# Optimization experiments

Hardware: AMD Instinct MI355X
Metric: run time of the kernel (lower is better)

## Reference

```python
import jax, jax.numpy as jnp
import numpy as np

CROSS_SIZES = [256, 256, 256]  # split_half=True -> carried field sizes [39,128,128,256]


def setup_inputs() -> dict:
    key = jax.random.key(0)
    ks = jax.random.split(key, 6)
    B, F, D = 1024, 39, 32
    scale = 0.05
    return {
        "x": jax.random.normal(ks[0], (B, F, D), dtype=jnp.float32),
        "W0": jax.random.normal(ks[1], (F * F, 256), dtype=jnp.float32) * scale,
        "b0": jnp.zeros((256,), dtype=jnp.float32),
        "W1": jax.random.normal(ks[2], (F * 128, 256), dtype=jnp.float32) * scale,
        "b1": jnp.zeros((256,), dtype=jnp.float32),
        "W2": jax.random.normal(ks[3], (F * 128, 256), dtype=jnp.float32) * scale,
        "b2": jnp.zeros((256,), dtype=jnp.float32),
        "fc_w": jax.random.normal(ks[4], (512, 1), dtype=jnp.float32) * scale,
        "fc_b": jnp.zeros((1,), dtype=jnp.float32),
    }


def reference(x, W0, b0, W1, b1, W2, b2, fc_w, fc_b):
    # x: (B, F, D)
    B, F, D = x.shape
    params = [(W0, b0), (W1, b1), (W2, b2)]
    n_layers = len(params)
    x0 = x
    h = x            # carried state, (B, Hi, D)
    finals = []
    for i, (W, b) in enumerate(params):
        Hp = h.shape[1]
        # per-embedding-dim outer product of fields, flattened: (B, D, F*Hp)
        z = jnp.einsum('bfd,bhd->bdfh', x0, h).reshape(B, D, F * Hp)
        # conv1d with kernel width 1 == dense projection over the F*Hp axis
        out = jax.nn.relu(z @ W + b)          # (B, D, O)
        out = jnp.transpose(out, (0, 2, 1))   # (B, O, D)
        if i != n_layers - 1:
            half = CROSS_SIZES[i] // 2
            h = out[:, :half]        # next_tmp (first half)
            finals.append(out[:, half:])  # h (second half)
        else:
            finals.append(out)
    res = jnp.concatenate(finals, axis=1)  # (B, 512, D)
    res = jnp.sum(res, axis=-1)            # (B, 512)
    return res @ fc_w + fc_b               # (B, 1)
```

## Files before the change

### kernel.cpp

```cpp
#include <hip/hip_runtime.h>
#include <stdint.h>


typedef unsigned int u32;
typedef unsigned short u16;
typedef __attribute__((ext_vector_type(8))) unsigned short us8;
typedef __attribute__((ext_vector_type(8))) _Float16 half8;
typedef __attribute__((ext_vector_type(4))) float f32x4;

__device__ __forceinline__ u16 f32_to_f16u(float f) {
  union { _Float16 h; u16 u; } c;
  c.h = (_Float16)f;
  return c.u;
}
__device__ __forceinline__ u32 pkmul(u32 a, u32 b) {
  u32 r;
  asm("v_pk_mul_f16 %0, %1, %2" : "=v"(r) : "v"(a), "v"(b));
  return r;
}
__device__ __forceinline__ void gload16(const u16* g, u16* l) {
  __builtin_amdgcn_global_load_lds((const __attribute__((address_space(1))) u32*)g,
                                   (__attribute__((address_space(3))) u32*)l, 16, 0, 0);
}
__device__ __forceinline__ void wait_vm4() {
  asm volatile("s_waitcnt vmcnt(4)" ::: "memory");
  __builtin_amdgcn_sched_barrier(0);
}
__device__ __forceinline__ void wait_vm0() {
  asm volatile("s_waitcnt vmcnt(0)" ::: "memory");
  __builtin_amdgcn_sched_barrier(0);
}

__global__ void prep_wt(const float* __restrict__ W0, const float* __restrict__ W1,
                        const float* __restrict__ W2, u16* __restrict__ WT0,
                        u16* __restrict__ WT1, u16* __restrict__ WT2) {
  int blk = blockIdx.x;
  const float* W;
  u16* WT;
  int KPAD, kp0;
  bool l0 = false;
  if (blk < 312) { W = W0; WT = WT0; KPAD = 2496; kp0 = blk * 8; l0 = true; }
  else if (blk < 936) { W = W1; WT = WT1; KPAD = 4992; kp0 = (blk - 312) * 8; }
  else { W = W2; WT = WT2; KPAD = 4992; kp0 = (blk - 936) * 8; }

  __shared__ u16 lds[8][257];
  int t = threadIdx.x;
  #pragma unroll
  for (int kk = 0; kk < 8; ++kk) {
    int kp = kp0 + kk;
    float v;
    if (l0) {
      int f = kp >> 6, hh = kp & 63;
      v = (hh < 39) ? W[(f * 39 + hh) * 256 + t] : 0.f;
    } else {
      v = W[kp * 256 + t];
    }
    lds[kk][t] = f32_to_f16u(v);
  }
  __syncthreads();
  us8 o;
  #pragma unroll
  for (int kk = 0; kk < 8; ++kk) o[kk] = lds[kk][t];
  *(us8*)(&WT[(size_t)t * KPAD + kp0]) = o;
}

template <int LAYER>
__global__ __launch_bounds__(512, 2) void cin_layer(
    const float* __restrict__ x, const u16* __restrict__ hin,
    const u16* __restrict__ WT, const float* __restrict__ bias,
    u16* __restrict__ hout, float* __restrict__ fsum) {
  constexpr int HPAD = (LAYER == 0) ? 64 : 128;
  constexpr int HROW = HPAD + 8;
  constexpr int KPAD = 39 * HPAD;
  constexpr int HC2 = HPAD / 64;
  constexpr int NT = 39 * HC2;

  __shared__ __align__(16) u16 wtile[2][256 * 64];
  __shared__ __align__(16) u16 hT[4][32][HROW];
  __shared__ u32 x0pk[4][32][41];

  const int tid = threadIdx.x;
  const int bbase = blockIdx.x * 4;

  for (int idx = tid; idx < 4 * 1248; idx += 512) {
    int b = idx / 1248;
    int rem = idx - b * 1248;
    int f = rem >> 5, d = rem & 31;
    u16 xh = f32_to_f16u(x[(bbase + b) * 1248 + rem]);
    x0pk[b][d][f] = (u32)xh | ((u32)xh << 16);
    if (LAYER == 0) hT[b][d][f] = xh;
  }
  if (LAYER == 0) {
    for (int idx = tid; idx < 4 * 32 * 25; idx += 512) {
      int b = idx / 800;
      int rem = idx - b * 800;
      int d = rem / 25, p = rem - d * 25;
      hT[b][d][39 + p] = 0;
    }
  } else {
    for (int idx = tid; idx < 4 * 32 * 16; idx += 512) {
      int b = idx >> 9, rem = idx & 511;
      int d = rem >> 4, c = rem & 15;
      us8 v = *(const us8*)(&hin[(((bbase + b) * 32 + d) << 7) + c * 8]);
      *(us8*)(&hT[b][d][c * 8]) = v;
    }
  }

  const int lane = tid & 63;
  const int w = tid >> 6;
  const int l15 = lane & 15;
  const int g = lane >> 4;

  const int nloc = lane >> 3, slot = lane & 7;
  const int qq = slot ^ nloc;
  const int cp = qq >> 2, kcp = qq & 3;
  const u16* wsrc = WT + (size_t)(w * 32 + nloc) * KPAD + cp * 32 + kcp * 8;

  const int xorm = (l15 & 7) * 8;
  const int rB0 = (w * 32 + l15) * 64;

  f32x4 acc[8][2];
  #pragma unroll
  for (int m = 0; m < 8; ++m)
    #pragma unroll
    for (int n = 0; n < 2; ++n) acc[m][n] = (f32x4){0.f, 0.f, 0.f, 0.f};

  {
    u16* dst = &wtile[0][(w * 32) * 64];
    #pragma unroll
    for (int j = 0; j < 4; ++j) gload16(wsrc + (size_t)j * 8 * KPAD, dst + j * 8 * 64);
  }
  __syncthreads();

  union HF { u32 u[4]; half8 h; us8 s; };
  int tt = 0;
  for (int t = 0; t < HC2; ++t) {
    HF hf2[8][2];
    #pragma unroll
    for (int m = 0; m < 8; ++m)
      #pragma unroll
      for (int c = 0; c < 2; ++c)
        hf2[m][c].s = *(const us8*)(&hT[m >> 1][(m & 1) * 16 + l15][(2 * t + c) * 32 + g * 8]);
    for (int f = 0; f < 39; ++f, ++tt) {
      const int buf = tt & 1;
      const bool more = (tt + 1 < NT);
      if (more) {
        const int nf = (f + 1 < 39) ? f + 1 : 0;
        const int ntp = (f + 1 < 39) ? t : t + 1;
        const int koff = nf * HPAD + ntp * 64;
        u16* dst = &wtile[buf ^ 1][(w * 32) * 64];
        #pragma unroll
        for (int j = 0; j < 4; ++j)
          gload16(wsrc + (size_t)j * 8 * KPAD + koff, dst + j * 8 * 64);
        wait_vm4();
      } else {
        wait_vm0();
      }
      u32 xs[8];
      #pragma unroll
      for (int m = 0; m < 8; ++m) xs[m] = x0pk[m >> 1][(m & 1) * 16 + l15][f];
      #pragma unroll
      for (int c = 0; c < 2; ++c) {
        const int off = (c * 32 + g * 8) ^ xorm;
        HF b0, b1;
        b0.s = *(const us8*)(&wtile[buf][rB0 + off]);
        b1.s = *(const us8*)(&wtile[buf][rB0 + 16 * 64 + off]);
        #pragma unroll
        for (int m = 0; m < 8; ++m) {
          HF a;
          #pragma unroll
          for (int i = 0; i < 4; ++i) a.u[i] = pkmul(hf2[m][c].u[i], xs[m]);
          acc[m][0] = __builtin_amdgcn_mfma_f32_16x16x32_f16(a.h, b0.h, acc[m][0], 0, 0, 0);
          acc[m][1] = __builtin_amdgcn_mfma_f32_16x16x32_f16(a.h, b1.h, acc[m][1], 0, 0, 0);
        }
      }
    }
  }

  float bv[2];
  #pragma unroll
  for (int nt = 0; nt < 2; ++nt) bv[nt] = bias[w * 32 + nt * 16 + l15];

  if (LAYER < 2 && w < 4) {
    #pragma unroll
    for (int m = 0; m < 8; ++m)
      #pragma unroll
      for (int nt = 0; nt < 2; ++nt) {
        int o = w * 32 + nt * 16 + l15;
        #pragma unroll
        for (int r = 0; r < 4; ++r) {
          int row = m * 16 + g * 4 + r;
          int s = row >> 5, d = row & 31;
          float v = fmaxf(acc[m][nt][r] + bv[nt], 0.f);
          hout[(((bbase + s) * 32 + d) << 7) + o] = f32_to_f16u(v);
        }
      }
  } else {
    #pragma unroll
    for (int nt = 0; nt < 2; ++nt) {
      float sub[4] = {0.f, 0.f, 0.f, 0.f};
      #pragma unroll
      for (int m = 0; m < 8; ++m)
        #pragma unroll
        for (int r = 0; r < 4; ++r)
          sub[m >> 1] += fmaxf(acc[m][nt][r] + bv[nt], 0.f);
      #pragma unroll
      for (int s = 0; s < 4; ++s) {
        sub[s] += __shfl_xor(sub[s], 16);
        sub[s] += __shfl_xor(sub[s], 32);
      }
      if (lane < 16) {
        int o = w * 32 + nt * 16 + l15;
        int j = (LAYER == 0) ? (o - 128) : ((LAYER == 1) ? o : (256 + o));
        #pragma unroll
        for (int s = 0; s < 4; ++s) fsum[(bbase + s) * 512 + j] = sub[s];
      }
    }
  }
}

__global__ void finalize(const float* __restrict__ fsum, const float* __restrict__ fc_w,
                         const float* __restrict__ fc_b, float* __restrict__ out) {
  int b = blockIdx.x;
  int lane = threadIdx.x;
  const float* fs = fsum + (size_t)b * 512;
  float s = 0.f;
  #pragma unroll
  for (int k = 0; k < 8; ++k) {
    int j = k * 64 + lane;
    s += fs[j] * fc_w[j];
  }
  #pragma unroll
  for (int off = 32; off; off >>= 1) s += __shfl_xor(s, off);
  if (lane == 0) out[b] = s + fc_b[0];
}

extern "C" void kernel_launch(void* const* d_in, const int* in_sizes, int n_in,
                              void* d_out, int out_size, void* d_ws, size_t ws_size,
                              hipStream_t stream) {
  const float* x = (const float*)d_in[0];
  const float* W0 = (const float*)d_in[1];
  const float* b0 = (const float*)d_in[2];
  const float* W1 = (const float*)d_in[3];
  const float* b1 = (const float*)d_in[4];
  const float* W2 = (const float*)d_in[5];
  const float* b2 = (const float*)d_in[6];
  const float* fc_w = (const float*)d_in[7];
  const float* fc_b = (const float*)d_in[8];
  float* out = (float*)d_out;

  char* ws = (char*)d_ws;
  size_t oWT0 = 0;
  size_t oWT1 = oWT0 + (size_t)256 * 2496 * 2;
  size_t oWT2 = oWT1 + (size_t)256 * 4992 * 2;
  size_t oH = oWT2 + (size_t)256 * 4992 * 2;
  size_t oFS = oH + (size_t)1024 * 32 * 128 * 2;
  u16* WT0 = (u16*)(ws + oWT0);
  u16* WT1 = (u16*)(ws + oWT1);
  u16* WT2 = (u16*)(ws + oWT2);
  u16* hbuf = (u16*)(ws + oH);
  float* fsum = (float*)(ws + oFS);

  prep_wt<<<1560, 256, 0, stream>>>(W0, W1, W2, WT0, WT1, WT2);
  cin_layer<0><<<256, 512, 0, stream>>>(x, nullptr, WT0, b0, hbuf, fsum);
  cin_layer<1><<<256, 512, 0, stream>>>(x, hbuf, WT1, b1, hbuf, fsum);
  cin_layer<2><<<256, 512, 0, stream>>>(x, hbuf, WT2, b2, nullptr, fsum);
  finalize<<<1024, 64, 0, stream>>>(fsum, fc_w, fc_b, out);
}
```

Before: 200.2 us.

## Halve batch per block, double the grid, and read carried state from global

Each CIN layer block now handles 2 batch samples instead of 4, so the grid grows to 512 blocks and launch bounds allow 4 waves per EU, meaning two blocks per CU. The LDS staging tile for the carried state is dropped. Layer 0 builds its A fragments from the packed x0 tile, and layers 1 and 2 load them straight from global memory into registers. A barrier is added before the in-place hout writes, so no wave can overwrite rows another wave still needs to read. The aim is better occupancy and latency hiding, at the cost of each weight tile being streamed twice as often, with half the MFMA reuse per loaded tile.

```diff
diff --git a/kernel.cpp b/kernel.cpp
--- a/kernel.cpp
+++ b/kernel.cpp
@@ -65,45 +65,27 @@
 }
 
 template <int LAYER>
-__global__ __launch_bounds__(512, 2) void cin_layer(
+__global__ __launch_bounds__(512, 4) void cin_layer(
     const float* __restrict__ x, const u16* __restrict__ hin,
     const u16* __restrict__ WT, const float* __restrict__ bias,
     u16* __restrict__ hout, float* __restrict__ fsum) {
   constexpr int HPAD = (LAYER == 0) ? 64 : 128;
-  constexpr int HROW = HPAD + 8;
   constexpr int KPAD = 39 * HPAD;
   constexpr int HC2 = HPAD / 64;
   constexpr int NT = 39 * HC2;
 
   __shared__ __align__(16) u16 wtile[2][256 * 64];
-  __shared__ __align__(16) u16 hT[4][32][HROW];
-  __shared__ u32 x0pk[4][32][41];
+  __shared__ u32 x0pk[2][32][41];
 
   const int tid = threadIdx.x;
-  const int bbase = blockIdx.x * 4;
-
-  for (int idx = tid; idx < 4 * 1248; idx += 512) {
+  const int bbase = blockIdx.x * 2;
+
+  for (int idx = tid; idx < 2 * 1248; idx += 512) {
     int b = idx / 1248;
     int rem = idx - b * 1248;
     int f = rem >> 5, d = rem & 31;
     u16 xh = f32_to_f16u(x[(bbase + b) * 1248 + rem]);
     x0pk[b][d][f] = (u32)xh | ((u32)xh << 16);
-    if (LAYER == 0) hT[b][d][f] = xh;
-  }
-  if (LAYER == 0) {
-    for (int idx = tid; idx < 4 * 32 * 25; idx += 512) {
-      int b = idx / 800;
-      int rem = idx - b * 800;
-      int d = rem / 25, p = rem - d * 25;
-      hT[b][d][39 + p] = 0;
-    }
-  } else {
-    for (int idx = tid; idx < 4 * 32 * 16; idx += 512) {
-      int b = idx >> 9, rem = idx & 511;
-      int d = rem >> 4, c = rem & 15;
-      us8 v = *(const us8*)(&hin[(((bbase + b) * 32 + d) << 7) + c * 8]);
-      *(us8*)(&hT[b][d][c * 8]) = v;
-    }
   }
 
   const int lane = tid & 63;
@@ -111,17 +93,24 @@
   const int l15 = lane & 15;
   const int g = lane >> 4;
 
+  int rs[4], rd[4];
+  #pragma unroll
+  for (int m = 0; m < 4; ++m) {
+    int row = m * 16 + l15;
+    rs[m] = row >> 5;
+    rd[m] = row & 31;
+  }
+
   const int nloc = lane >> 3, slot = lane & 7;
   const int qq = slot ^ nloc;
-  const int cp = qq >> 2, kcp = qq & 3;
-  const u16* wsrc = WT + (size_t)(w * 32 + nloc) * KPAD + cp * 32 + kcp * 8;
+  const u16* wsrc = WT + (size_t)(w * 32 + nloc) * KPAD + qq * 8;
 
   const int xorm = (l15 & 7) * 8;
   const int rB0 = (w * 32 + l15) * 64;
 
-  f32x4 acc[8][2];
-  #pragma unroll
-  for (int m = 0; m < 8; ++m)
+  f32x4 acc[4][2];
+  #pragma unroll
+  for (int m = 0; m < 4; ++m)
     #pragma unroll
     for (int n = 0; n < 2; ++n) acc[m][n] = (f32x4){0.f, 0.f, 0.f, 0.f};
 
@@ -135,12 +124,27 @@
   union HF { u32 u[4]; half8 h; us8 s; };
   int tt = 0;
   for (int t = 0; t < HC2; ++t) {
-    HF hf2[8][2];
-    #pragma unroll
-    for (int m = 0; m < 8; ++m)
-      #pragma unroll
-      for (int c = 0; c < 2; ++c)
-        hf2[m][c].s = *(const us8*)(&hT[m >> 1][(m & 1) * 16 + l15][(2 * t + c) * 32 + g * 8]);
+    HF hf2[4][2];
+    if (LAYER == 0) {
+      #pragma unroll
+      for (int m = 0; m < 4; ++m)
+        #pragma unroll
+        for (int c = 0; c < 2; ++c)
+          #pragma unroll
+          for (int i = 0; i < 4; ++i) {
+            int h0 = c * 32 + g * 8 + 2 * i;
+            u32 lo = (h0 < 39) ? (x0pk[rs[m]][rd[m]][h0] & 0xffffu) : 0u;
+            u32 hi = (h0 + 1 < 39) ? (x0pk[rs[m]][rd[m]][h0 + 1] & 0xffffu) : 0u;
+            hf2[m][c].u[i] = lo | (hi << 16);
+          }
+    } else {
+      #pragma unroll
+      for (int m = 0; m < 4; ++m)
+        #pragma unroll
+        for (int c = 0; c < 2; ++c)
+          hf2[m][c].s = *(const us8*)(
+              &hin[(((size_t)(bbase + rs[m]) * 32 + rd[m]) << 7) + (2 * t + c) * 32 + g * 8]);
+    }
     for (int f = 0; f < 39; ++f, ++tt) {
       const int buf = tt & 1;
       const bool more = (tt + 1 < NT);
@@ -156,9 +160,9 @@
       } else {
         wait_vm0();
       }
-      u32 xs[8];
-      #pragma unroll
-      for (int m = 0; m < 8; ++m) xs[m] = x0pk[m >> 1][(m & 1) * 16 + l15][f];
+      u32 xs[4];
+      #pragma unroll
+      for (int m = 0; m < 4; ++m) xs[m] = x0pk[rs[m]][rd[m]][f];
       #pragma unroll
       for (int c = 0; c < 2; ++c) {
         const int off = (c * 32 + g * 8) ^ xorm;
@@ -166,7 +170,7 @@
         b0.s = *(const us8*)(&wtile[buf][rB0 + off]);
         b1.s = *(const us8*)(&wtile[buf][rB0 + 16 * 64 + off]);
         #pragma unroll
-        for (int m = 0; m < 8; ++m) {
+        for (int m = 0; m < 4; ++m) {
           HF a;
           #pragma unroll
           for (int i = 0; i < 4; ++i) a.u[i] = pkmul(hf2[m][c].u[i], xs[m]);
@@ -177,13 +181,15 @@
     }
   }
 
+  __syncthreads();
+
   float bv[2];
   #pragma unroll
   for (int nt = 0; nt < 2; ++nt) bv[nt] = bias[w * 32 + nt * 16 + l15];
 
   if (LAYER < 2 && w < 4) {
     #pragma unroll
-    for (int m = 0; m < 8; ++m)
+    for (int m = 0; m < 4; ++m)
       #pragma unroll
       for (int nt = 0; nt < 2; ++nt) {
         int o = w * 32 + nt * 16 + l15;
@@ -198,22 +204,22 @@
   } else {
     #pragma unroll
     for (int nt = 0; nt < 2; ++nt) {
-      float sub[4] = {0.f, 0.f, 0.f, 0.f};
-      #pragma unroll
-      for (int m = 0; m < 8; ++m)
+      float sub[2] = {0.f, 0.f};
+      #pragma unroll
+      for (int m = 0; m < 4; ++m)
         #pragma unroll
         for (int r = 0; r < 4; ++r)
           sub[m >> 1] += fmaxf(acc[m][nt][r] + bv[nt], 0.f);
       #pragma unroll
-      for (int s = 0; s < 4; ++s) {
+      for (int s = 0; s < 2; ++s) {
         sub[s] += __shfl_xor(sub[s], 16);
         sub[s] += __shfl_xor(sub[s], 32);
       }
       if (lane < 16) {
         int o = w * 32 + nt * 16 + l15;
         int j = (LAYER == 0) ? (o - 128) : ((LAYER == 1) ? o : (256 + o));
-        #pragma unroll
-        for (int s = 0; s < 4; ++s) fsum[(bbase + s) * 512 + j] = sub[s];
+        fsum[(bbase + 0) * 512 + j] = sub[0];
+        fsum[(bbase + 1) * 512 + j] = sub[1];
       }
     }
   }
@@ -262,8 +268,8 @@
   float* fsum = (float*)(ws + oFS);
 
   prep_wt<<<1560, 256, 0, stream>>>(W0, W1, W2, WT0, WT1, WT2);
-  cin_layer<0><<<256, 512, 0, stream>>>(x, nullptr, WT0, b0, hbuf, fsum);
-  cin_layer<1><<<256, 512, 0, stream>>>(x, hbuf, WT1, b1, hbuf, fsum);
-  cin_layer<2><<<256, 512, 0, stream>>>(x, hbuf, WT2, b2, nullptr, fsum);
+  cin_layer<0><<<512, 512, 0, stream>>>(x, nullptr, WT0, b0, hbuf, fsum);
+  cin_layer<1><<<512, 512, 0, stream>>>(x, hbuf, WT1, b1, hbuf, fsum);
+  cin_layer<2><<<512, 512, 0, stream>>>(x, hbuf, WT2, b2, nullptr, fsum);
   finalize<<<1024, 64, 0, stream>>>(fsum, fc_w, fc_b, out);
 }
```

Result: slower. 226.7 us (+13.2%).

## Software-pipeline weight fragment loads ahead of MFMA in CIN layer loop

Applied to the files above, without the earlier changes.

Restructures the main K loop into a single flat loop that holds register-prefetched weight fragments and x0 values for the current step. The next tile's global-to-LDS load is issued first, then MFMAs run on registers, and only afterwards does it wait on vmcnt(0) and read the next fragments. This hides LDS read latency and the global load behind compute instead of waiting before the MFMAs. It also simplifies the wsrc offset computation. There is no __syncthreads between iterations, but each wave writes and reads only its own rows of the tile, so this looks safe. Register pressure rises because of the extra fragment registers.

```diff
diff --git a/kernel.cpp b/kernel.cpp
--- a/kernel.cpp
+++ b/kernel.cpp
@@ -22,11 +22,7 @@
   __builtin_amdgcn_global_load_lds((const __attribute__((address_space(1))) u32*)g,
                                    (__attribute__((address_space(3))) u32*)l, 16, 0, 0);
 }
-__device__ __forceinline__ void wait_vm4() {
-  asm volatile("s_waitcnt vmcnt(4)" ::: "memory");
-  __builtin_amdgcn_sched_barrier(0);
-}
-__device__ __forceinline__ void wait_vm0() {
+__device__ __forceinline__ void wait_vm0_sb() {
   asm volatile("s_waitcnt vmcnt(0)" ::: "memory");
   __builtin_amdgcn_sched_barrier(0);
 }
@@ -113,8 +109,7 @@
 
   const int nloc = lane >> 3, slot = lane & 7;
   const int qq = slot ^ nloc;
-  const int cp = qq >> 2, kcp = qq & 3;
-  const u16* wsrc = WT + (size_t)(w * 32 + nloc) * KPAD + cp * 32 + kcp * 8;
+  const u16* wsrc = WT + (size_t)(w * 32 + nloc) * KPAD + qq * 8;
 
   const int xorm = (l15 & 7) * 8;
   const int rB0 = (w * 32 + l15) * 64;
@@ -133,47 +128,70 @@
   __syncthreads();
 
   union HF { u32 u[4]; half8 h; us8 s; };
-  int tt = 0;
-  for (int t = 0; t < HC2; ++t) {
-    HF hf2[8][2];
-    #pragma unroll
-    for (int m = 0; m < 8; ++m)
-      #pragma unroll
-      for (int c = 0; c < 2; ++c)
-        hf2[m][c].s = *(const us8*)(&hT[m >> 1][(m & 1) * 16 + l15][(2 * t + c) * 32 + g * 8]);
-    for (int f = 0; f < 39; ++f, ++tt) {
-      const int buf = tt & 1;
-      const bool more = (tt + 1 < NT);
-      if (more) {
-        const int nf = (f + 1 < 39) ? f + 1 : 0;
-        const int ntp = (f + 1 < 39) ? t : t + 1;
-        const int koff = nf * HPAD + ntp * 64;
-        u16* dst = &wtile[buf ^ 1][(w * 32) * 64];
-        #pragma unroll
-        for (int j = 0; j < 4; ++j)
-          gload16(wsrc + (size_t)j * 8 * KPAD + koff, dst + j * 8 * 64);
-        wait_vm4();
-      } else {
-        wait_vm0();
-      }
-      u32 xs[8];
-      #pragma unroll
-      for (int m = 0; m < 8; ++m) xs[m] = x0pk[m >> 1][(m & 1) * 16 + l15][f];
+
+  HF hf2[8][2];
+  #pragma unroll
+  for (int m = 0; m < 8; ++m)
+    #pragma unroll
+    for (int c = 0; c < 2; ++c)
+      hf2[m][c].s = *(const us8*)(&hT[m >> 1][(m & 1) * 16 + l15][c * 32 + g * 8]);
+
+  HF fr[2][2];
+  u32 xs[8];
+  #pragma unroll
+  for (int c = 0; c < 2; ++c) {
+    const int off = (c * 32 + g * 8) ^ xorm;
+    fr[c][0].s = *(const us8*)(&wtile[0][rB0 + off]);
+    fr[c][1].s = *(const us8*)(&wtile[0][rB0 + 16 * 64 + off]);
+  }
+  #pragma unroll
+  for (int m = 0; m < 8; ++m) xs[m] = x0pk[m >> 1][(m & 1) * 16 + l15][0];
+
+  int f = 0, hc = 0;
+  for (int tt = 0; tt < NT; ++tt) {
+    const int buf = tt & 1;
+    const bool more = (tt + 1 < NT);
+    int nf = f + 1, nhc = hc;
+    if (nf == 39) { nf = 0; ++nhc; }
+    if (more) {
+      const int koff = nf * HPAD + nhc * 64;
+      u16* dst = &wtile[buf ^ 1][(w * 32) * 64];
+      #pragma unroll
+      for (int j = 0; j < 4; ++j)
+        gload16(wsrc + (size_t)j * 8 * KPAD + koff, dst + j * 8 * 64);
+      __builtin_amdgcn_sched_barrier(0);
+    }
+    #pragma unroll
+    for (int c = 0; c < 2; ++c) {
+      #pragma unroll
+      for (int m = 0; m < 8; ++m) {
+        HF a;
+        #pragma unroll
+        for (int i = 0; i < 4; ++i) a.u[i] = pkmul(hf2[m][c].u[i], xs[m]);
+        acc[m][0] = __builtin_amdgcn_mfma_f32_16x16x32_f16(a.h, fr[c][0].h, acc[m][0], 0, 0, 0);
+        acc[m][1] = __builtin_amdgcn_mfma_f32_16x16x32_f16(a.h, fr[c][1].h, acc[m][1], 0, 0, 0);
+      }
+    }
+    if (more) {
+      wait_vm0_sb();
       #pragma unroll
       for (int c = 0; c < 2; ++c) {
         const int off = (c * 32 + g * 8) ^ xorm;
-        HF b0, b1;
-        b0.s = *(const us8*)(&wtile[buf][rB0 + off]);
-        b1.s = *(const us8*)(&wtile[buf][rB0 + 16 * 64 + off]);
-        #pragma unroll
-        for (int m = 0; m < 8; ++m) {
-          HF a;
+        fr[c][0].s = *(const us8*)(&wtile[buf ^ 1][rB0 + off]);
+        fr[c][1].s = *(const us8*)(&wtile[buf ^ 1][rB0 + 16 * 64 + off]);
+      }
+      #pragma unroll
+      for (int m = 0; m < 8; ++m) xs[m] = x0pk[m >> 1][(m & 1) * 16 + l15][nf];
+      if (nhc != hc) {
+        #pragma unroll
+        for (int m = 0; m < 8; ++m)
           #pragma unroll
-          for (int i = 0; i < 4; ++i) a.u[i] = pkmul(hf2[m][c].u[i], xs[m]);
-          acc[m][0] = __builtin_amdgcn_mfma_f32_16x16x32_f16(a.h, b0.h, acc[m][0], 0, 0, 0);
-          acc[m][1] = __builtin_amdgcn_mfma_f32_16x16x32_f16(a.h, b1.h, acc[m][1], 0, 0, 0);
-        }
-      }
+          for (int c = 0; c < 2; ++c)
+            hf2[m][c].s =
+                *(const us8*)(&hT[m >> 1][(m & 1) * 16 + l15][(2 * nhc + c) * 32 + g * 8]);
+      }
+      f = nf;
+      hc = nhc;
     }
   }
 
```

Result: no change. 201.3 us (+0.5%).

## Switch CIN layer GEMM from 16x16x32 to 32x32x16 MFMA tiles

Applied to the files above, without the earlier changes.

Replaces the 16x16x32 f16 MFMA tiling (8x2 accumulators per wave) with 32x32x16 MFMA (4 accumulators of 16 floats). Each row tile now covers one batch sample's 32 embedding dims. The hidden-state fragments and weight-tile swizzle are reworked to match, and the nested loops are flattened into a single tile loop that reloads h fragments only when the H chunk changes. The intent is fewer A-operand pk_mul instructions per MFMA FLOP and fewer LDS B reads, at the cost of a different LDS access pattern and new epilogue index mapping.

```diff
diff --git a/kernel.cpp b/kernel.cpp
--- a/kernel.cpp
+++ b/kernel.cpp
@@ -6,7 +6,7 @@
 typedef unsigned short u16;
 typedef __attribute__((ext_vector_type(8))) unsigned short us8;
 typedef __attribute__((ext_vector_type(8))) _Float16 half8;
-typedef __attribute__((ext_vector_type(4))) float f32x4;
+typedef __attribute__((ext_vector_type(16))) float f32x16;
 
 __device__ __forceinline__ u16 f32_to_f16u(float f) {
   union { _Float16 h; u16 u; } c;
@@ -108,22 +108,21 @@
 
   const int lane = tid & 63;
   const int w = tid >> 6;
-  const int l15 = lane & 15;
-  const int g = lane >> 4;
+  const int l31 = lane & 31;
+  const int hi = lane >> 5;
 
   const int nloc = lane >> 3, slot = lane & 7;
   const int qq = slot ^ nloc;
-  const int cp = qq >> 2, kcp = qq & 3;
-  const u16* wsrc = WT + (size_t)(w * 32 + nloc) * KPAD + cp * 32 + kcp * 8;
-
-  const int xorm = (l15 & 7) * 8;
-  const int rB0 = (w * 32 + l15) * 64;
-
-  f32x4 acc[8][2];
-  #pragma unroll
-  for (int m = 0; m < 8; ++m)
-    #pragma unroll
-    for (int n = 0; n < 2; ++n) acc[m][n] = (f32x4){0.f, 0.f, 0.f, 0.f};
+  const u16* wsrc = WT + (size_t)(w * 32 + nloc) * KPAD + qq * 8;
+
+  const int rB = (w * 32 + l31) * 64;
+  const int r7 = l31 & 7;
+
+  f32x16 acc[4];
+  #pragma unroll
+  for (int m = 0; m < 4; ++m)
+    #pragma unroll
+    for (int r = 0; r < 16; ++r) acc[m][r] = 0.f;
 
   {
     u16* dst = &wtile[0][(w * 32) * 64];
@@ -133,87 +132,79 @@
   __syncthreads();
 
   union HF { u32 u[4]; half8 h; us8 s; };
-  int tt = 0;
-  for (int t = 0; t < HC2; ++t) {
-    HF hf2[8][2];
-    #pragma unroll
-    for (int m = 0; m < 8; ++m)
-      #pragma unroll
-      for (int c = 0; c < 2; ++c)
-        hf2[m][c].s = *(const us8*)(&hT[m >> 1][(m & 1) * 16 + l15][(2 * t + c) * 32 + g * 8]);
-    for (int f = 0; f < 39; ++f, ++tt) {
-      const int buf = tt & 1;
-      const bool more = (tt + 1 < NT);
-      if (more) {
-        const int nf = (f + 1 < 39) ? f + 1 : 0;
-        const int ntp = (f + 1 < 39) ? t : t + 1;
-        const int koff = nf * HPAD + ntp * 64;
-        u16* dst = &wtile[buf ^ 1][(w * 32) * 64];
+
+  HF hf2[4][4];
+  #pragma unroll
+  for (int m = 0; m < 4; ++m)
+    #pragma unroll
+    for (int kk = 0; kk < 4; ++kk)
+      hf2[m][kk].s = *(const us8*)(&hT[m][l31][kk * 16 + hi * 8]);
+
+  int f = 0, hc = 0;
+  for (int tt = 0; tt < NT; ++tt) {
+    const int buf = tt & 1;
+    const bool more = (tt + 1 < NT);
+    int nf = f + 1, nhc = hc;
+    if (nf == 39) { nf = 0; ++nhc; }
+    if (more) {
+      const int koff = nf * HPAD + nhc * 64;
+      u16* dst = &wtile[buf ^ 1][(w * 32) * 64];
+      #pragma unroll
+      for (int j = 0; j < 4; ++j)
+        gload16(wsrc + (size_t)j * 8 * KPAD + koff, dst + j * 8 * 64);
+      wait_vm4();
+    } else {
+      wait_vm0();
+    }
+    u32 xs[4];
+    #pragma unroll
+    for (int m = 0; m < 4; ++m) xs[m] = x0pk[m][l31][f];
+    #pragma unroll
+    for (int kk = 0; kk < 4; ++kk) {
+      HF b;
+      b.s = *(const us8*)(&wtile[buf][rB + (((kk * 2 + hi) ^ r7) * 8)]);
+      #pragma unroll
+      for (int m = 0; m < 4; ++m) {
+        HF a;
         #pragma unroll
-        for (int j = 0; j < 4; ++j)
-          gload16(wsrc + (size_t)j * 8 * KPAD + koff, dst + j * 8 * 64);
-        wait_vm4();
-      } else {
-        wait_vm0();
+        for (int i = 0; i < 4; ++i) a.u[i] = pkmul(hf2[m][kk].u[i], xs[m]);
+        acc[m] = __builtin_amdgcn_mfma_f32_32x32x16_f16(a.h, b.h, acc[m], 0, 0, 0);
       }
-      u32 xs[8];
-      #pragma unroll
-      for (int m = 0; m < 8; ++m) xs[m] = x0pk[m >> 1][(m & 1) * 16 + l15][f];
-      #pragma unroll
-      for (int c = 0; c < 2; ++c) {
-        const int off = (c * 32 + g * 8) ^ xorm;
-        HF b0, b1;
-        b0.s = *(const us8*)(&wtile[buf][rB0 + off]);
-        b1.s = *(const us8*)(&wtile[buf][rB0 + 16 * 64 + off]);
+    }
+    if (more && nhc != hc) {
+      #pragma unroll
+      for (int m = 0; m < 4; ++m)
         #pragma unroll
-        for (int m = 0; m < 8; ++m) {
-          HF a;
-          #pragma unroll
-          for (int i = 0; i < 4; ++i) a.u[i] = pkmul(hf2[m][c].u[i], xs[m]);
-          acc[m][0] = __builtin_amdgcn_mfma_f32_16x16x32_f16(a.h, b0.h, acc[m][0], 0, 0, 0);
-          acc[m][1] = __builtin_amdgcn_mfma_f32_16x16x32_f16(a.h, b1.h, acc[m][1], 0, 0, 0);
-        }
-      }
-    }
-  }
-
-  float bv[2];
-  #pragma unroll
-  for (int nt = 0; nt < 2; ++nt) bv[nt] = bias[w * 32 + nt * 16 + l15];
+        for (int kk = 0; kk < 4; ++kk)
+          hf2[m][kk].s = *(const us8*)(&hT[m][l31][nhc * 64 + kk * 16 + hi * 8]);
+    }
+    f = nf;
+    hc = nhc;
+  }
+
+  const float bv = bias[w * 32 + l31];
 
   if (LAYER < 2 && w < 4) {
-    #pragma unroll
-    for (int m = 0; m < 8; ++m)
-      #pragma unroll
-      for (int nt = 0; nt < 2; ++nt) {
-        int o = w * 32 + nt * 16 + l15;
-        #pragma unroll
-        for (int r = 0; r < 4; ++r) {
-          int row = m * 16 + g * 4 + r;
-          int s = row >> 5, d = row & 31;
-          float v = fmaxf(acc[m][nt][r] + bv[nt], 0.f);
-          hout[(((bbase + s) * 32 + d) << 7) + o] = f32_to_f16u(v);
-        }
+    const int o = w * 32 + l31;
+    #pragma unroll
+    for (int m = 0; m < 4; ++m)
+      #pragma unroll
+      for (int r = 0; r < 16; ++r) {
+        int d = (r & 3) + 8 * (r >> 2) + 4 * hi;
+        float v = fmaxf(acc[m][r] + bv, 0.f);
+        hout[(((bbase + m) * 32 + d) << 7) + o] = f32_to_f16u(v);
       }
   } else {
     #pragma unroll
-    for (int nt = 0; nt < 2; ++nt) {
-      float sub[4] = {0.f, 0.f, 0.f, 0.f};
-      #pragma unroll
-      for (int m = 0; m < 8; ++m)
-        #pragma unroll
-        for (int r = 0; r < 4; ++r)
-          sub[m >> 1] += fmaxf(acc[m][nt][r] + bv[nt], 0.f);
-      #pragma unroll
-      for (int s = 0; s < 4; ++s) {
-        sub[s] += __shfl_xor(sub[s], 16);
-        sub[s] += __shfl_xor(sub[s], 32);
-      }
-      if (lane < 16) {
-        int o = w * 32 + nt * 16 + l15;
+    for (int m = 0; m < 4; ++m) {
+      float sub = 0.f;
+      #pragma unroll
+      for (int r = 0; r < 16; ++r) sub += fmaxf(acc[m][r] + bv, 0.f);
+      sub += __shfl_xor(sub, 32);
+      if (lane < 32) {
+        int o = w * 32 + l31;
         int j = (LAYER == 0) ? (o - 128) : ((LAYER == 1) ? o : (256 + o));
-        #pragma unroll
-        for (int s = 0; s < 4; ++s) fsum[(bbase + s) * 512 + j] = sub[s];
+        fsum[(bbase + m) * 512 + j] = sub;
       }
     }
   }
```

New measurement: 221.4 us. 1.11x slower.
